# Kernel tuning notes

Hardware: AMD Instinct MI355X
Metric: run time of the kernel (lower is better)

The kernel has to match this reference:

```python
import jax, jax.numpy as jnp
import numpy as np

K = 512          # num_embeddings
D = 64           # embedding_dim
BETA = 0.25      # commitment_cost
DECAY = 0.99
EPS = 1e-5


def setup_inputs() -> dict:
    key = jax.random.key(0)
    k1, k2, k3 = jax.random.split(key, 3)
    inputs = jax.random.normal(k1, (64, D, 32, 32), dtype=jnp.float32)  # NCHW, C == embedding_dim
    embedding = jax.random.normal(k2, (K, D), dtype=jnp.float32)
    ema_w = jax.random.normal(k3, (K, D), dtype=jnp.float32)
    ema_cluster_size = jnp.zeros((K,), dtype=jnp.float32)
    return {"inputs": inputs, "embedding": embedding, "ema_w": ema_w,
            "ema_cluster_size": ema_cluster_size}


def reference(inputs, embedding, ema_w, ema_cluster_size):
    # NCHW -> NHWC, flatten to [N, D]
    x = jnp.transpose(inputs, (0, 2, 3, 1))
    B, H, W, C = x.shape
    flat = x.reshape(-1, C)                                   # [N, D]

    # squared L2 distances to all codes: [N, K]
    d = (jnp.sum(flat * flat, axis=1, keepdims=True)
         + jnp.sum(embedding * embedding, axis=1)
         - 2.0 * flat @ embedding.T)
    idx = jnp.argmin(d, axis=1)                               # [N]

    # gather (equivalent to one-hot @ embedding, without materializing one-hot)
    quantized = embedding[idx].reshape(x.shape)               # [B,H,W,D]

    # EMA codebook update (training branch); segment sums replace encodings.T matmuls
    counts = jax.ops.segment_sum(jnp.ones_like(idx, dtype=flat.dtype), idx,
                                 num_segments=K)              # [K]
    new_cs = ema_cluster_size * DECAY + (1.0 - DECAY) * counts
    n = jnp.sum(new_cs)
    new_cs = (new_cs + EPS) / (n + K * EPS) * n               # Laplace smoothing
    dw = jax.ops.segment_sum(flat, idx, num_segments=K)       # [K, D]
    new_ema_w = ema_w * DECAY + (1.0 - DECAY) * dw
    new_embedding = new_ema_w / new_cs[:, None]

    # commitment loss + straight-through estimator
    e_latent_loss = jnp.mean((jax.lax.stop_gradient(quantized) - x) ** 2)
    loss = BETA * e_latent_loss
    quantized_st = x + jax.lax.stop_gradient(quantized - x)

    avg_probs = counts / flat.shape[0]
    perplexity = jnp.exp(-jnp.sum(avg_probs * jnp.log(avg_probs + 1e-10)))

    out_q = jnp.transpose(quantized_st, (0, 3, 1, 2))         # back to NCHW
    return (loss, out_q, perplexity, idx.reshape(B, H, W),
            new_cs, new_ema_w, new_embedding)
```

## Files before the change

### kernel.cpp

```cpp
#include <hip/hip_runtime.h>

#define K_CODES 512
#define DIM 64
#define HW 1024
#define NVEC 65536
#define NREP 4

#define O0 0
#define O1 1
#define O2 4194305
#define O3 4194306
#define O4 4259842
#define O5 4260354
#define O6 4293122

#define WS_EE   0
#define WS_CNT  512
#define WS_LOSS 2560
#define WS_DW   4608
#define WS_BP   135680

typedef __bf16 bf16x8 __attribute__((ext_vector_type(8)));
typedef float  f32x4  __attribute__((ext_vector_type(4)));

__global__ void k0_init(const float* __restrict__ emb, float* __restrict__ wsf) {
    const int b = blockIdx.x, t = threadIdx.x;
    if (b < 512) {
        wsf[WS_DW + b * 256 + t] = 0.0f;
    } else if (b == 512) {
        int* cnt = (int*)(wsf + WS_CNT);
        #pragma unroll
        for (int i = 0; i < 8; ++i) cnt[i * 256 + t] = 0;
    } else if (b < 515) {
        int k = (b - 513) * 256 + t;
        const float* e = emb + k * DIM;
        float s = 0.0f;
        #pragma unroll
        for (int c = 0; c < DIM; ++c) s += e[c] * e[c];
        wsf[WS_EE + k] = s;
    } else {
        int g = (b - 515) * 256 + t;
        int j    = g & 7;
        int lane = (g >> 3) & 63;
        int ks   = (g >> 9) & 1;
        int rest = g >> 10;
        int ntg  = rest & 31;
        int s    = rest >> 5;
        int code = ntg * 16 + (lane & 15);
        int c    = ks * 32 + (lane >> 4) * 8 + j;
        float v = -2.0f * emb[code * DIM + c];
        __bf16 h0 = (__bf16)v;  float r1 = v  - (float)h0;
        __bf16 h1 = (__bf16)r1; float r2 = r1 - (float)h1;
        __bf16 hv = (s == 0) ? h0 : (s == 1 ? h1 : (__bf16)r2);
        ((__bf16*)(wsf + WS_BP))[g] = hv;
    }
}

__global__ __launch_bounds__(256, 4)
void k1_main(const float* __restrict__ in, const float* __restrict__ emb,
             float* __restrict__ out, float* __restrict__ wsf) {
    __shared__ float xs[32 * 65];
    __shared__ unsigned int xsp[3][32 * 36];
    __shared__ float pmin[4][32];
    __shared__ int   pidx[4][32];
    __shared__ float xxs[32];
    __shared__ int   hist[K_CODES];

    const int t    = threadIdx.x;
    const int lane = t & 63;
    const int wave = t >> 6;
    const int ni   = wave;
    const int col  = lane & 15;
    const int quad = lane >> 4;

    hist[t] = 0; hist[t + 256] = 0;

    const int blk     = blockIdx.x;
    const int rep     = blk & (NREP - 1);
    const int n_img   = blk >> 5;
    const int hw_base = (blk & 31) * 32;
    const float* xbase = in + n_img * (DIM * HW) + hw_base;

    #pragma unroll
    for (int it = 0; it < 8; ++it) {
        int e = it * 256 + t;
        int c = e >> 5, h = e & 31;
        xs[h * 65 + c] = xbase[c * HW + h];
    }

    f32x4 acc[2][8];
    #pragma unroll
    for (int nt = 0; nt < 8; ++nt) {
        float eev = wsf[WS_EE + ni * 128 + nt * 16 + col];
        #pragma unroll
        for (int mi = 0; mi < 2; ++mi) {
            acc[mi][nt][0] = eev; acc[mi][nt][1] = eev;
            acc[mi][nt][2] = eev; acc[mi][nt][3] = eev;
        }
    }

    __syncthreads();

    #pragma unroll
    for (int i = 0; i < 4; ++i) {
        int e = i * 256 + t;
        int row = e >> 5, cp = e & 31;
        float v0 = xs[row * 65 + 2 * cp];
        float v1 = xs[row * 65 + 2 * cp + 1];
        __bf16 a0 = (__bf16)v0; float ra = v0 - (float)a0;
        __bf16 a1 = (__bf16)ra; ra -= (float)a1;
        __bf16 a2 = (__bf16)ra;
        __bf16 b0 = (__bf16)v1; float rb = v1 - (float)b0;
        __bf16 b1 = (__bf16)rb; rb -= (float)b1;
        __bf16 b2 = (__bf16)rb;
        union { __bf16 h[2]; unsigned int u; } u0, u1, u2;
        u0.h[0] = a0; u0.h[1] = b0;
        u1.h[0] = a1; u1.h[1] = b1;
        u2.h[0] = a2; u2.h[1] = b2;
        xsp[0][row * 36 + cp] = u0.u;
        xsp[1][row * 36 + cp] = u1.u;
        xsp[2][row * 36 + cp] = u2.u;
    }
    if (t < 32) {
        float s = 0.0f;
        #pragma unroll
        for (int c = 0; c < DIM; ++c) { float v = xs[t * 65 + c]; s += v * v; }
        xxs[t] = s;
    }
    __syncthreads();

    const bf16x8* bp8 = (const bf16x8*)(wsf + WS_BP);

    #pragma unroll
    for (int ks = 0; ks < 2; ++ks) {
        bf16x8 A0[2], A1[2], A2[2];
        #pragma unroll
        for (int mi = 0; mi < 2; ++mi) {
            int u = (mi * 16 + col) * 36 + ks * 16 + quad * 4;
            A0[mi] = *(const bf16x8*)&xsp[0][u];
            A1[mi] = *(const bf16x8*)&xsp[1][u];
            A2[mi] = *(const bf16x8*)&xsp[2][u];
        }
        #pragma unroll
        for (int s = 0; s < 3; ++s) {
            #pragma unroll
            for (int bh = 0; bh < 2; ++bh) {
                bf16x8 Bv[4];
                #pragma unroll
                for (int n4 = 0; n4 < 4; ++n4) {
                    int nt = bh * 4 + n4;
                    Bv[n4] = bp8[(((s * 32 + ni * 8 + nt) * 2 + ks) * 64) + lane];
                }
                #pragma unroll
                for (int mi = 0; mi < 2; ++mi)
                    #pragma unroll
                    for (int n4 = 0; n4 < 4; ++n4)
                        acc[mi][bh * 4 + n4] = __builtin_amdgcn_mfma_f32_16x16x32_bf16(A0[mi], Bv[n4], acc[mi][bh * 4 + n4], 0, 0, 0);
                if (s < 2) {
                    #pragma unroll
                    for (int mi = 0; mi < 2; ++mi)
                        #pragma unroll
                        for (int n4 = 0; n4 < 4; ++n4)
                            acc[mi][bh * 4 + n4] = __builtin_amdgcn_mfma_f32_16x16x32_bf16(A1[mi], Bv[n4], acc[mi][bh * 4 + n4], 0, 0, 0);
                }
                if (s == 0) {
                    #pragma unroll
                    for (int mi = 0; mi < 2; ++mi)
                        #pragma unroll
                        for (int n4 = 0; n4 < 4; ++n4)
                            acc[mi][bh * 4 + n4] = __builtin_amdgcn_mfma_f32_16x16x32_bf16(A2[mi], Bv[n4], acc[mi][bh * 4 + n4], 0, 0, 0);
                }
            }
        }
    }

    #pragma unroll
    for (int mi = 0; mi < 2; ++mi) {
        #pragma unroll
        for (int r = 0; r < 4; ++r) {
            float v  = acc[mi][0][r];
            int   bi = ni * 128 + col;
            #pragma unroll
            for (int nt = 1; nt < 8; ++nt) {
                float u  = acc[mi][nt][r];
                int   ui = ni * 128 + nt * 16 + col;
                if (u < v) { v = u; bi = ui; }
            }
            #pragma unroll
            for (int off = 1; off < 16; off <<= 1) {
                float ov = __shfl_xor(v, off);
                int   oi = __shfl_xor(bi, off);
                if (ov < v || (ov == v && oi < bi)) { v = ov; bi = oi; }
            }
            if (col == 0) {
                int row = mi * 16 + quad * 4 + r;
                pmin[ni][row] = v;
                pidx[ni][row] = bi;
            }
        }
    }
    __syncthreads();

    if (t < 32) {
        float v = pmin[0][t]; int bi = pidx[0][t];
        #pragma unroll
        for (int q = 1; q < 4; ++q) {
            float u = pmin[q][t]; int ui = pidx[q][t];
            if (u < v) { v = u; bi = ui; }
        }
        pidx[0][t] = bi;
        out[O3 + blk * 32 + t] = (float)bi;
        atomicAdd(&hist[bi], 1);
        float ld = v + xxs[t];
        #pragma unroll
        for (int off = 16; off > 0; off >>= 1) ld += __shfl_down(ld, off);
        if (t == 0) wsf[WS_LOSS + blk] = ld;
    }
    __syncthreads();

    {
        int v = t & 31, cq = t >> 5;
        int kv = pidx[0][v];
        const float* ew = emb + kv * DIM;
        float* oq = out + O1 + n_img * (DIM * HW) + hw_base + v;
        #pragma unroll
        for (int c = cq * 8; c < cq * 8 + 8; ++c) oq[c * HW] = ew[c];
    }

    {
        float* dw = wsf + WS_DW + rep * 32768;
        #pragma unroll 1
        for (int v = wave * 8; v < wave * 8 + 8; ++v) {
            int kv = pidx[0][v];
            atomicAdd(&dw[kv * DIM + lane], xs[v * 65 + lane]);
        }
    }

    int* cnt = (int*)(wsf + WS_CNT);
    if (hist[t])       atomicAdd(&cnt[rep * 512 + t], hist[t]);
    if (hist[t + 256]) atomicAdd(&cnt[rep * 512 + t + 256], hist[t + 256]);
}

__global__ void k2(const float* __restrict__ ema_cs, const float* __restrict__ ema_w,
                   float* __restrict__ out, const float* __restrict__ wsf) {
    __shared__ float s1[256], s2[256];
    const int t = threadIdx.x;
    const int blk = blockIdx.x;
    const int* cnt = (const int*)(wsf + WS_CNT);

    float ca = 0.0f, cb = 0.0f;
    #pragma unroll
    for (int r = 0; r < NREP; ++r) {
        ca += (float)cnt[r * 512 + t];
        cb += (float)cnt[r * 512 + 256 + t];
    }
    float ra = 0.99f * ema_cs[t]       + 0.01f * ca;
    float rb = 0.99f * ema_cs[256 + t] + 0.01f * cb;
    float pa = ca * (1.0f / 65536.0f);
    float pb = cb * (1.0f / 65536.0f);
    s1[t] = ra + rb;
    s2[t] = pa * logf(pa + 1e-10f) + pb * logf(pb + 1e-10f);
    __syncthreads();
    for (int s = 128; s > 0; s >>= 1) {
        if (t < s) { s1[t] += s1[t + s]; s2[t] += s2[t + s]; }
        __syncthreads();
    }
    const float n = s1[0];
    const float den = n + 512.0f * 1e-5f;

    {
        int m = blk * 256 + t;
        int k = m >> 6;
        float dwsum = wsf[WS_DW + m] + wsf[WS_DW + 32768 + m]
                    + wsf[WS_DW + 65536 + m] + wsf[WS_DW + 98304 + m];
        float w = 0.99f * ema_w[m] + 0.01f * dwsum;
        float ck = 0.0f;
        #pragma unroll
        for (int r = 0; r < NREP; ++r) ck += (float)cnt[r * 512 + k];
        float rawk = 0.99f * ema_cs[k] + 0.01f * ck;
        float csk = (rawk + 1e-5f) / den * n;
        out[O5 + m] = w;
        out[O6 + m] = w / csk;
    }

    if (blk == 0) {
        float s2v = s2[0];
        out[O4 + t]       = (ra + 1e-5f) / den * n;
        out[O4 + 256 + t] = (rb + 1e-5f) / den * n;
        __syncthreads();
        float lsum = 0.0f;
        #pragma unroll
        for (int j = 0; j < 8; ++j) lsum += wsf[WS_LOSS + j * 256 + t];
        s1[t] = lsum;
        __syncthreads();
        for (int s = 128; s > 0; s >>= 1) {
            if (t < s) s1[t] += s1[t + s];
            __syncthreads();
        }
        if (t == 0) {
            out[O0] = 0.25f * s1[0] * (1.0f / 4194304.0f);
            out[O2] = expf(-s2v);
        }
    }
}

extern "C" void kernel_launch(void* const* d_in, const int* in_sizes, int n_in,
                              void* d_out, int out_size, void* d_ws, size_t ws_size,
                              hipStream_t stream) {
    const float* in     = (const float*)d_in[0];
    const float* emb    = (const float*)d_in[1];
    const float* ema_w  = (const float*)d_in[2];
    const float* ema_cs = (const float*)d_in[3];
    float* out = (float*)d_out;
    float* wsf = (float*)d_ws;

    hipLaunchKernelGGL(k0_init, dim3(899),  dim3(256), 0, stream, emb, wsf);
    hipLaunchKernelGGL(k1_main, dim3(2048), dim3(256), 0, stream, in, emb, out, wsf);
    hipLaunchKernelGGL(k2,      dim3(128),  dim3(256), 0, stream, ema_cs, ema_w, out, wsf);
}
```

Before: 137.1 us.

## Replace atomic dw scatter with per-code gather over stored flat vectors

The fp32 atomicAdd scatter of input vectors into replicated dw buckets is removed from the main kernel. The main kernel now writes each transposed flat vector to workspace, and the final kernel launches one block per code. Each block scans all 65536 indices to build a list of matching vectors, then sums those rows. The goal is to avoid atomic contention and the dw zeroing pass, at the cost of a 16MB extra write/read and every block scanning the full index array. The count also comes from the list length, and n is precomputed in the init kernel. The LISTCAP of 12288 caps the list, so a code assigned more vectors than that gets a truncated sum and count.

```diff
diff --git a/kernel.cpp b/kernel.cpp
--- a/kernel.cpp
+++ b/kernel.cpp
@@ -17,29 +17,39 @@
 #define WS_EE   0
 #define WS_CNT  512
 #define WS_LOSS 2560
-#define WS_DW   4608
-#define WS_BP   135680
+#define WS_N    4608
+#define WS_FLAT 4864
+#define WS_BP   4199168
+
+#define LISTCAP 12288
 
 typedef __bf16 bf16x8 __attribute__((ext_vector_type(8)));
 typedef float  f32x4  __attribute__((ext_vector_type(4)));
 
-__global__ void k0_init(const float* __restrict__ emb, float* __restrict__ wsf) {
+__global__ void k0_init(const float* __restrict__ emb, const float* __restrict__ ema_cs,
+                        float* __restrict__ wsf) {
+    __shared__ float sn[256];
     const int b = blockIdx.x, t = threadIdx.x;
-    if (b < 512) {
-        wsf[WS_DW + b * 256 + t] = 0.0f;
-    } else if (b == 512) {
+    if (b == 0) {
         int* cnt = (int*)(wsf + WS_CNT);
         #pragma unroll
         for (int i = 0; i < 8; ++i) cnt[i * 256 + t] = 0;
-    } else if (b < 515) {
-        int k = (b - 513) * 256 + t;
+        sn[t] = ema_cs[t] + ema_cs[t + 256];
+        __syncthreads();
+        for (int s = 128; s > 0; s >>= 1) {
+            if (t < s) sn[t] += sn[t + s];
+            __syncthreads();
+        }
+        if (t == 0) wsf[WS_N] = 0.99f * sn[0] + 0.01f * 65536.0f;
+    } else if (b < 3) {
+        int k = (b - 1) * 256 + t;
         const float* e = emb + k * DIM;
         float s = 0.0f;
         #pragma unroll
         for (int c = 0; c < DIM; ++c) s += e[c] * e[c];
         wsf[WS_EE + k] = s;
     } else {
-        int g = (b - 515) * 256 + t;
+        int g = (b - 3) * 256 + t;
         int j    = g & 7;
         int lane = (g >> 3) & 63;
         int ks   = (g >> 9) & 1;
@@ -126,6 +136,12 @@
         #pragma unroll
         for (int c = 0; c < DIM; ++c) { float v = xs[t * 65 + c]; s += v * v; }
         xxs[t] = s;
+    }
+
+    #pragma unroll
+    for (int v8 = 0; v8 < 8; ++v8) {
+        int v = wave * 8 + v8;
+        wsf[WS_FLAT + (blk * 32 + v) * 64 + lane] = xs[v * 65 + lane];
     }
     __syncthreads();
 
@@ -227,15 +243,6 @@
         for (int c = cq * 8; c < cq * 8 + 8; ++c) oq[c * HW] = ew[c];
     }
 
-    {
-        float* dw = wsf + WS_DW + rep * 32768;
-        #pragma unroll 1
-        for (int v = wave * 8; v < wave * 8 + 8; ++v) {
-            int kv = pidx[0][v];
-            atomicAdd(&dw[kv * DIM + lane], xs[v * 65 + lane]);
-        }
-    }
-
     int* cnt = (int*)(wsf + WS_CNT);
     if (hist[t])       atomicAdd(&cnt[rep * 512 + t], hist[t]);
     if (hist[t + 256]) atomicAdd(&cnt[rep * 512 + t + 256], hist[t + 256]);
@@ -243,64 +250,81 @@
 
 __global__ void k2(const float* __restrict__ ema_cs, const float* __restrict__ ema_w,
                    float* __restrict__ out, const float* __restrict__ wsf) {
+    __shared__ int   list[LISTCAP];
+    __shared__ int   lcnt;
+    __shared__ float rpart[4][64];
     __shared__ float s1[256], s2[256];
+
     const int t = threadIdx.x;
+    const int lane = t & 63;
+    const int w = t >> 6;
     const int blk = blockIdx.x;
-    const int* cnt = (const int*)(wsf + WS_CNT);
-
-    float ca = 0.0f, cb = 0.0f;
-    #pragma unroll
-    for (int r = 0; r < NREP; ++r) {
-        ca += (float)cnt[r * 512 + t];
-        cb += (float)cnt[r * 512 + 256 + t];
-    }
-    float ra = 0.99f * ema_cs[t]       + 0.01f * ca;
-    float rb = 0.99f * ema_cs[256 + t] + 0.01f * cb;
-    float pa = ca * (1.0f / 65536.0f);
-    float pb = cb * (1.0f / 65536.0f);
-    s1[t] = ra + rb;
-    s2[t] = pa * logf(pa + 1e-10f) + pb * logf(pb + 1e-10f);
-    __syncthreads();
-    for (int s = 128; s > 0; s >>= 1) {
-        if (t < s) { s1[t] += s1[t + s]; s2[t] += s2[t + s]; }
-        __syncthreads();
-    }
-    const float n = s1[0];
-    const float den = n + 512.0f * 1e-5f;
-
-    {
-        int m = blk * 256 + t;
-        int k = m >> 6;
-        float dwsum = wsf[WS_DW + m] + wsf[WS_DW + 32768 + m]
-                    + wsf[WS_DW + 65536 + m] + wsf[WS_DW + 98304 + m];
-        float w = 0.99f * ema_w[m] + 0.01f * dwsum;
-        float ck = 0.0f;
-        #pragma unroll
-        for (int r = 0; r < NREP; ++r) ck += (float)cnt[r * 512 + k];
-        float rawk = 0.99f * ema_cs[k] + 0.01f * ck;
-        float csk = (rawk + 1e-5f) / den * n;
-        out[O5 + m] = w;
-        out[O6 + m] = w / csk;
-    }
-
-    if (blk == 0) {
-        float s2v = s2[0];
-        out[O4 + t]       = (ra + 1e-5f) / den * n;
-        out[O4 + 256 + t] = (rb + 1e-5f) / den * n;
-        __syncthreads();
-        float lsum = 0.0f;
-        #pragma unroll
-        for (int j = 0; j < 8; ++j) lsum += wsf[WS_LOSS + j * 256 + t];
-        s1[t] = lsum;
+
+    if (blk == 512) {
+        float ls = 0.0f;
+        #pragma unroll
+        for (int j = 0; j < 8; ++j) ls += wsf[WS_LOSS + j * 256 + t];
+        s1[t] = ls;
+        const int* cnt = (const int*)(wsf + WS_CNT);
+        float ca = 0.0f, cb = 0.0f;
+        #pragma unroll
+        for (int r = 0; r < NREP; ++r) {
+            ca += (float)cnt[r * 512 + t];
+            cb += (float)cnt[r * 512 + 256 + t];
+        }
+        float pa = ca * (1.0f / 65536.0f);
+        float pb = cb * (1.0f / 65536.0f);
+        s2[t] = pa * logf(pa + 1e-10f) + pb * logf(pb + 1e-10f);
         __syncthreads();
         for (int s = 128; s > 0; s >>= 1) {
-            if (t < s) s1[t] += s1[t + s];
+            if (t < s) { s1[t] += s1[t + s]; s2[t] += s2[t + s]; }
             __syncthreads();
         }
         if (t == 0) {
             out[O0] = 0.25f * s1[0] * (1.0f / 4194304.0f);
-            out[O2] = expf(-s2v);
-        }
+            out[O2] = expf(-s2[0]);
+        }
+        return;
+    }
+
+    const int k = blk;
+    if (t == 0) lcnt = 0;
+    __syncthreads();
+
+    const float fk = (float)k;
+    const float* idxf = out + O3;
+    #pragma unroll 4
+    for (int i = 0; i < 256; ++i) {
+        int v = i * 256 + t;
+        float f = idxf[v];
+        if (f == fk) {
+            int p = atomicAdd(&lcnt, 1);
+            if (p < LISTCAP) list[p] = v;
+        }
+    }
+    __syncthreads();
+    int m = lcnt < LISTCAP ? lcnt : LISTCAP;
+
+    const float* flat = wsf + WS_FLAT;
+    float a[4] = {0.0f, 0.0f, 0.0f, 0.0f};
+    for (int i = w * 4; i < m; i += 16) {
+        #pragma unroll
+        for (int j = 0; j < 4; ++j)
+            if (i + j < m) a[j] += flat[list[i + j] * 64 + lane];
+    }
+    rpart[w][lane] = (a[0] + a[1]) + (a[2] + a[3]);
+    __syncthreads();
+
+    if (t < 64) {
+        float dwv = rpart[0][t] + rpart[1][t] + rpart[2][t] + rpart[3][t];
+        float countk = (float)m;
+        float raw = 0.99f * ema_cs[k] + 0.01f * countk;
+        float n   = wsf[WS_N];
+        float cs  = (raw + 1e-5f) / (n + 512.0f * 1e-5f) * n;
+        float wv  = 0.99f * ema_w[k * DIM + t] + 0.01f * dwv;
+        out[O5 + k * DIM + t] = wv;
+        out[O6 + k * DIM + t] = wv / cs;
+        if (t == 0) out[O4 + k] = cs;
     }
 }
 
@@ -314,7 +338,7 @@
     float* out = (float*)d_out;
     float* wsf = (float*)d_ws;
 
-    hipLaunchKernelGGL(k0_init, dim3(899),  dim3(256), 0, stream, emb, wsf);
+    hipLaunchKernelGGL(k0_init, dim3(387),  dim3(256), 0, stream, emb, ema_cs, wsf);
     hipLaunchKernelGGL(k1_main, dim3(2048), dim3(256), 0, stream, in, emb, out, wsf);
-    hipLaunchKernelGGL(k2,      dim3(128),  dim3(256), 0, stream, ema_cs, ema_w, out, wsf);
+    hipLaunchKernelGGL(k2,      dim3(513),  dim3(256), 0, stream, ema_cs, ema_w, out, wsf);
 }
```

Result: slower. 320.0 us (+133.4%).

## Drop fp32 staging tile, double atomic replicas, precompute cluster-size sum

Applied to the files above, without the earlier changes.

The main kernel now splits input values straight from global memory into the bf16 triple-split shared buffers and no longer stages an fp32 transposed tile. Per-thread partial sums feed the squared norms, and one barrier is removed. The dw scatter rebuilds each fp32 value from the three bf16 pieces, which may not be bit-exact. Atomic replicas for counts and dw grow from 4 to 8 to reduce contention, and the EMA cluster-size total n is computed in the init kernel from the known total count. This lets the finalize kernel skip its per-block reduction and move loss and perplexity into a separate block. The global input loads now read 32 consecutive floats per channel per warp slice, which may be less coalesced than before.

```diff
diff --git a/kernel.cpp b/kernel.cpp
--- a/kernel.cpp
+++ b/kernel.cpp
@@ -4,7 +4,7 @@
 #define DIM 64
 #define HW 1024
 #define NVEC 65536
-#define NREP 4
+#define NREP 8
 
 #define O0 0
 #define O1 1
@@ -16,30 +16,44 @@
 
 #define WS_EE   0
 #define WS_CNT  512
-#define WS_LOSS 2560
-#define WS_DW   4608
-#define WS_BP   135680
+#define WS_LOSS 4608
+#define WS_N    6656
+#define WS_DW   6912
+#define WS_BP   269056
 
 typedef __bf16 bf16x8 __attribute__((ext_vector_type(8)));
 typedef float  f32x4  __attribute__((ext_vector_type(4)));
 
-__global__ void k0_init(const float* __restrict__ emb, float* __restrict__ wsf) {
+union U2 { unsigned int u; unsigned short us[2]; __bf16 h[2]; };
+
+__global__ void k0_init(const float* __restrict__ emb, const float* __restrict__ ema_cs,
+                        float* __restrict__ wsf) {
+    __shared__ float sn[256];
     const int b = blockIdx.x, t = threadIdx.x;
-    if (b < 512) {
-        wsf[WS_DW + b * 256 + t] = 0.0f;
-    } else if (b == 512) {
+    if (b < 128) {
+        #pragma unroll
+        for (int i = 0; i < 8; ++i)
+            wsf[WS_DW + b * 2048 + i * 256 + t] = 0.0f;
+    } else if (b == 128) {
         int* cnt = (int*)(wsf + WS_CNT);
         #pragma unroll
-        for (int i = 0; i < 8; ++i) cnt[i * 256 + t] = 0;
-    } else if (b < 515) {
-        int k = (b - 513) * 256 + t;
+        for (int i = 0; i < 16; ++i) cnt[i * 256 + t] = 0;
+        sn[t] = ema_cs[t] + ema_cs[t + 256];
+        __syncthreads();
+        for (int s = 128; s > 0; s >>= 1) {
+            if (t < s) sn[t] += sn[t + s];
+            __syncthreads();
+        }
+        if (t == 0) wsf[WS_N] = 0.99f * sn[0] + 0.01f * 65536.0f;
+    } else if (b < 131) {
+        int k = (b - 129) * 256 + t;
         const float* e = emb + k * DIM;
         float s = 0.0f;
         #pragma unroll
         for (int c = 0; c < DIM; ++c) s += e[c] * e[c];
         wsf[WS_EE + k] = s;
     } else {
-        int g = (b - 515) * 256 + t;
+        int g = (b - 131) * 256 + t;
         int j    = g & 7;
         int lane = (g >> 3) & 63;
         int ks   = (g >> 9) & 1;
@@ -59,8 +73,8 @@
 __global__ __launch_bounds__(256, 4)
 void k1_main(const float* __restrict__ in, const float* __restrict__ emb,
              float* __restrict__ out, float* __restrict__ wsf) {
-    __shared__ float xs[32 * 65];
     __shared__ unsigned int xsp[3][32 * 36];
+    __shared__ float xxp[32][9];
     __shared__ float pmin[4][32];
     __shared__ int   pidx[4][32];
     __shared__ float xxs[32];
@@ -81,13 +95,6 @@
     const int hw_base = (blk & 31) * 32;
     const float* xbase = in + n_img * (DIM * HW) + hw_base;
 
-    #pragma unroll
-    for (int it = 0; it < 8; ++it) {
-        int e = it * 256 + t;
-        int c = e >> 5, h = e & 31;
-        xs[h * 65 + c] = xbase[c * HW + h];
-    }
-
     f32x4 acc[2][8];
     #pragma unroll
     for (int nt = 0; nt < 8; ++nt) {
@@ -99,35 +106,40 @@
         }
     }
 
+    {
+        const int h   = t & 31;
+        const int cp0 = t >> 5;
+        float xxa = 0.0f;
+        #pragma unroll
+        for (int it = 0; it < 4; ++it) {
+            int cp = it * 8 + cp0;
+            float v0 = xbase[(2 * cp) * HW + h];
+            float v1 = xbase[(2 * cp + 1) * HW + h];
+            __bf16 a0 = (__bf16)v0; float ra = v0 - (float)a0;
+            __bf16 a1 = (__bf16)ra; ra -= (float)a1;
+            __bf16 a2 = (__bf16)ra;
+            __bf16 b0 = (__bf16)v1; float rb = v1 - (float)b0;
+            __bf16 b1 = (__bf16)rb; rb -= (float)b1;
+            __bf16 b2 = (__bf16)rb;
+            U2 u0, u1, u2;
+            u0.h[0] = a0; u0.h[1] = b0;
+            u1.h[0] = a1; u1.h[1] = b1;
+            u2.h[0] = a2; u2.h[1] = b2;
+            xsp[0][h * 36 + cp] = u0.u;
+            xsp[1][h * 36 + cp] = u1.u;
+            xsp[2][h * 36 + cp] = u2.u;
+            xxa += v0 * v0 + v1 * v1;
+        }
+        xxp[h][cp0] = xxa;
+    }
     __syncthreads();
 
-    #pragma unroll
-    for (int i = 0; i < 4; ++i) {
-        int e = i * 256 + t;
-        int row = e >> 5, cp = e & 31;
-        float v0 = xs[row * 65 + 2 * cp];
-        float v1 = xs[row * 65 + 2 * cp + 1];
-        __bf16 a0 = (__bf16)v0; float ra = v0 - (float)a0;
-        __bf16 a1 = (__bf16)ra; ra -= (float)a1;
-        __bf16 a2 = (__bf16)ra;
-        __bf16 b0 = (__bf16)v1; float rb = v1 - (float)b0;
-        __bf16 b1 = (__bf16)rb; rb -= (float)b1;
-        __bf16 b2 = (__bf16)rb;
-        union { __bf16 h[2]; unsigned int u; } u0, u1, u2;
-        u0.h[0] = a0; u0.h[1] = b0;
-        u1.h[0] = a1; u1.h[1] = b1;
-        u2.h[0] = a2; u2.h[1] = b2;
-        xsp[0][row * 36 + cp] = u0.u;
-        xsp[1][row * 36 + cp] = u1.u;
-        xsp[2][row * 36 + cp] = u2.u;
-    }
     if (t < 32) {
         float s = 0.0f;
         #pragma unroll
-        for (int c = 0; c < DIM; ++c) { float v = xs[t * 65 + c]; s += v * v; }
+        for (int j = 0; j < 8; ++j) s += xxp[t][j];
         xxs[t] = s;
     }
-    __syncthreads();
 
     const bf16x8* bp8 = (const bf16x8*)(wsf + WS_BP);
 
@@ -228,11 +240,17 @@
     }
 
     {
-        float* dw = wsf + WS_DW + rep * 32768;
+        float* dwr = wsf + WS_DW + rep * 32768;
         #pragma unroll 1
-        for (int v = wave * 8; v < wave * 8 + 8; ++v) {
+        for (int v8 = 0; v8 < 8; ++v8) {
+            int v  = wave * 8 + v8;
             int kv = pidx[0][v];
-            atomicAdd(&dw[kv * DIM + lane], xs[v * 65 + lane]);
+            int wi = v * 36 + (lane >> 1);
+            U2 a0, a1, a2;
+            a0.u = xsp[0][wi]; a1.u = xsp[1][wi]; a2.u = xsp[2][wi];
+            int hs = lane & 1;
+            float val = (float)a0.h[hs] + (float)a1.h[hs] + (float)a2.h[hs];
+            atomicAdd(&dwr[kv * 64 + lane], val);
         }
     }
 
@@ -248,60 +266,47 @@
     const int blk = blockIdx.x;
     const int* cnt = (const int*)(wsf + WS_CNT);
 
-    float ca = 0.0f, cb = 0.0f;
+    if (blk == 128) {
+        float ls = 0.0f;
+        #pragma unroll
+        for (int j = 0; j < 8; ++j) ls += wsf[WS_LOSS + j * 256 + t];
+        s1[t] = ls;
+        float ca = 0.0f, cb = 0.0f;
+        #pragma unroll
+        for (int r = 0; r < NREP; ++r) {
+            ca += (float)cnt[r * 512 + t];
+            cb += (float)cnt[r * 512 + 256 + t];
+        }
+        float pa = ca * (1.0f / 65536.0f);
+        float pb = cb * (1.0f / 65536.0f);
+        s2[t] = pa * logf(pa + 1e-10f) + pb * logf(pb + 1e-10f);
+        __syncthreads();
+        for (int s = 128; s > 0; s >>= 1) {
+            if (t < s) { s1[t] += s1[t + s]; s2[t] += s2[t + s]; }
+            __syncthreads();
+        }
+        if (t == 0) {
+            out[O0] = 0.25f * s1[0] * (1.0f / 4194304.0f);
+            out[O2] = expf(-s2[0]);
+        }
+        return;
+    }
+
+    const int m = blk * 256 + t;
+    const int k = m >> 6;
+    float ck = 0.0f, dwsum = 0.0f;
     #pragma unroll
     for (int r = 0; r < NREP; ++r) {
-        ca += (float)cnt[r * 512 + t];
-        cb += (float)cnt[r * 512 + 256 + t];
-    }
-    float ra = 0.99f * ema_cs[t]       + 0.01f * ca;
-    float rb = 0.99f * ema_cs[256 + t] + 0.01f * cb;
-    float pa = ca * (1.0f / 65536.0f);
-    float pb = cb * (1.0f / 65536.0f);
-    s1[t] = ra + rb;
-    s2[t] = pa * logf(pa + 1e-10f) + pb * logf(pb + 1e-10f);
-    __syncthreads();
-    for (int s = 128; s > 0; s >>= 1) {
-        if (t < s) { s1[t] += s1[t + s]; s2[t] += s2[t + s]; }
-        __syncthreads();
-    }
-    const float n = s1[0];
-    const float den = n + 512.0f * 1e-5f;
-
-    {
-        int m = blk * 256 + t;
-        int k = m >> 6;
-        float dwsum = wsf[WS_DW + m] + wsf[WS_DW + 32768 + m]
-                    + wsf[WS_DW + 65536 + m] + wsf[WS_DW + 98304 + m];
-        float w = 0.99f * ema_w[m] + 0.01f * dwsum;
-        float ck = 0.0f;
-        #pragma unroll
-        for (int r = 0; r < NREP; ++r) ck += (float)cnt[r * 512 + k];
-        float rawk = 0.99f * ema_cs[k] + 0.01f * ck;
-        float csk = (rawk + 1e-5f) / den * n;
-        out[O5 + m] = w;
-        out[O6 + m] = w / csk;
-    }
-
-    if (blk == 0) {
-        float s2v = s2[0];
-        out[O4 + t]       = (ra + 1e-5f) / den * n;
-        out[O4 + 256 + t] = (rb + 1e-5f) / den * n;
-        __syncthreads();
-        float lsum = 0.0f;
-        #pragma unroll
-        for (int j = 0; j < 8; ++j) lsum += wsf[WS_LOSS + j * 256 + t];
-        s1[t] = lsum;
-        __syncthreads();
-        for (int s = 128; s > 0; s >>= 1) {
-            if (t < s) s1[t] += s1[t + s];
-            __syncthreads();
-        }
-        if (t == 0) {
-            out[O0] = 0.25f * s1[0] * (1.0f / 4194304.0f);
-            out[O2] = expf(-s2v);
-        }
-    }
+        ck    += (float)cnt[r * 512 + k];
+        dwsum += wsf[WS_DW + r * 32768 + m];
+    }
+    float n    = wsf[WS_N];
+    float rawk = 0.99f * ema_cs[k] + 0.01f * ck;
+    float csk  = (rawk + 1e-5f) / (n + 512.0f * 1e-5f) * n;
+    float wv   = 0.99f * ema_w[m] + 0.01f * dwsum;
+    out[O5 + m] = wv;
+    out[O6 + m] = wv / csk;
+    if ((m & 63) == 0) out[O4 + k] = csk;
 }
 
 extern "C" void kernel_launch(void* const* d_in, const int* in_sizes, int n_in,
@@ -314,7 +319,7 @@
     float* out = (float*)d_out;
     float* wsf = (float*)d_ws;
 
-    hipLaunchKernelGGL(k0_init, dim3(899),  dim3(256), 0, stream, emb, wsf);
+    hipLaunchKernelGGL(k0_init, dim3(515),  dim3(256), 0, stream, emb, ema_cs, wsf);
     hipLaunchKernelGGL(k1_main, dim3(2048), dim3(256), 0, stream, in, emb, out, wsf);
-    hipLaunchKernelGGL(k2,      dim3(128),  dim3(256), 0, stream, ema_cs, ema_w, out, wsf);
+    hipLaunchKernelGGL(k2,      dim3(129),  dim3(256), 0, stream, ema_cs, ema_w, out, wsf);
 }
```

Result: no change. 139.0 us (+1.4%).
